# Performance work log

Measured on AMD Instinct MI355X. Metric: run time of the kernel, lower is better.

The kernel has to match this reference:

```python
import jax, jax.numpy as jnp
import numpy as np

N = 100000        # nodes
E = 1600000       # edges (avg degree 16)
IN_DIM = 128
OUT_DIM = 128
P_DROP = 0.1


def setup_inputs() -> dict:
    key = jax.random.key(0)
    k1, k2, k3, k4 = jax.random.split(key, 4)
    x = jax.random.normal(k1, (N, IN_DIM), dtype=jnp.float32)
    edge_index = jax.random.randint(k2, (2, E), 0, N, dtype=jnp.int64)
    # glorot-uniform-ish init for the GCNConv linear weight
    limit = float(np.sqrt(6.0 / (IN_DIM + OUT_DIM)))
    W = jax.random.uniform(k3, (IN_DIM, OUT_DIM), dtype=jnp.float32,
                           minval=-limit, maxval=limit)
    b = jnp.zeros((OUT_DIM,), dtype=jnp.float32)
    drop_u = jax.random.uniform(k4, (N, OUT_DIM), dtype=jnp.float32)
    return {"x": x, "edge_index": edge_index, "W": W, "b": b, "drop_u": drop_u}


def reference(x, edge_index, W, b, drop_u):
    n = x.shape[0]
    # linear transform first (PyG GCNConv: lin has no bias)
    h = x @ W  # [N, OUT]
    # add self-loops
    loops = jnp.arange(n, dtype=edge_index.dtype)
    src = jnp.concatenate([edge_index[0], loops])  # [E+N]
    dst = jnp.concatenate([edge_index[1], loops])
    # symmetric normalization: deg computed on destination column
    deg = jax.ops.segment_sum(jnp.ones_like(dst, dtype=h.dtype), dst,
                              num_segments=n)
    dinv = jnp.where(deg > 0, jax.lax.rsqrt(deg), 0.0)
    norm = dinv[src] * dinv[dst]  # [E+N]
    # gather-message-scatter: out[dst] += norm * h[src]
    msgs = h[src] * norm[:, None]                       # [E+N, OUT]
    out = jax.ops.segment_sum(msgs, dst, num_segments=n) + b
    # ReLU + (deterministic-mask) inverted dropout
    out = jax.nn.relu(out)
    keep = 1.0 - P_DROP
    out = jnp.where(drop_u >= P_DROP, out / keep, 0.0)
    return out
```

## Files before the change

### kernel.cpp

```cpp
#include <hip/hip_runtime.h>

#define DIM 128
#define D4 32
#define D2 64
#define EPB1 4096

typedef short short8 __attribute__((ext_vector_type(8)));
typedef float f32x4 __attribute__((ext_vector_type(4)));

__device__ __forceinline__ unsigned pack_bf16(float a, float b) {
    unsigned ua = __float_as_uint(a);
    unsigned ub = __float_as_uint(b);
    ua = (ua + 0x7FFFu + ((ua >> 16) & 1u)) >> 16;
    ub = (ub + 0x7FFFu + ((ub >> 16) & 1u)) & 0xFFFF0000u;
    return ua | ub;
}
__device__ __forceinline__ unsigned short bf16_of(float a) {
    unsigned ua = __float_as_uint(a);
    return (unsigned short)((ua + 0x7FFFu + ((ua >> 16) & 1u)) >> 16);
}


__global__ __launch_bounds__(512) void k_hist1(const int* __restrict__ dst, int E,
                                               int* __restrict__ H, int* __restrict__ tot,
                                               int NB1, int NBUCK) {
    __shared__ int h[512];
    const int t = threadIdx.x;
    for (int i = t; i < NBUCK; i += 512) h[i] = 0;
    __syncthreads();
    const int base = blockIdx.x * EPB1;
#pragma unroll
    for (int i = 0; i < EPB1 / 512; ++i) {
        int e = base + i * 512 + t;
        if (e < E) atomicAdd(&h[dst[e] >> 9], 1);
    }
    __syncthreads();
    for (int i = t; i < NBUCK; i += 512) {
        int c = h[i];
        H[i * NB1 + blockIdx.x] = c;
        if (c) atomicAdd(&tot[i], c);
    }
}

__global__ __launch_bounds__(512) void k_scanA(const int* __restrict__ tot,
                                               int* __restrict__ binbase, int NBUCK) {
    __shared__ int sh[512];
    const int t = threadIdx.x;
    int v = (t < NBUCK) ? tot[t] : 0;
    sh[t] = v;
    __syncthreads();
    for (int o = 1; o < 512; o <<= 1) {
        int x = (t >= o) ? sh[t - o] : 0;
        __syncthreads();
        sh[t] += x;
        __syncthreads();
    }
    if (t < NBUCK) binbase[t] = sh[t] - v;
    if (t == NBUCK - 1) binbase[NBUCK] = sh[t];
}

__global__ __launch_bounds__(512) void k_scanB(int* __restrict__ H,
                                               const int* __restrict__ binbase, int NB1) {
    __shared__ int sh[512];
    const int bin = blockIdx.x;
    const int t = threadIdx.x;
    int v = (t < NB1) ? H[bin * NB1 + t] : 0;
    sh[t] = v;
    __syncthreads();
    for (int o = 1; o < 512; o <<= 1) {
        int x = (t >= o) ? sh[t - o] : 0;
        __syncthreads();
        sh[t] += x;
        __syncthreads();
    }
    if (t < NB1) H[bin * NB1 + t] = binbase[bin] + sh[t] - v;
}

__global__ __launch_bounds__(512) void k_scatter1(const int* __restrict__ ei, int E,
                                                  const int* __restrict__ H,
                                                  unsigned* __restrict__ ebuf,
                                                  int NB1, int NBUCK) {
    __shared__ int cnt[512];
    const int t = threadIdx.x;
    const int blk = blockIdx.x;
    for (int i = t; i < NBUCK; i += 512) cnt[i] = 0;
    __syncthreads();
    const int* src = ei;
    const int* dst = ei + E;
    const int base = blk * EPB1;
#pragma unroll
    for (int i = 0; i < EPB1 / 512; ++i) {
        int e = base + i * 512 + t;
        if (e < E) {
            int d = dst[e];
            int s = src[e];
            int b = d >> 9;
            int r = atomicAdd(&cnt[b], 1);
            ebuf[H[b * NB1 + blk] + r] = ((unsigned)s << 9) | (unsigned)(d & 511);
        }
    }
}

__global__ __launch_bounds__(512) void k_bucket2(const unsigned* __restrict__ ebuf,
                                                 const int* __restrict__ binbase,
                                                 int* __restrict__ srclist,
                                                 int* __restrict__ rowstart,
                                                 float* __restrict__ dinv,
                                                 int n, int E) {
    __shared__ int h[512];
    __shared__ int off[512];
    __shared__ int cnt[512];
    const int t = threadIdx.x;
    const int b = blockIdx.x;
    const int beg = binbase[b];
    const int end = binbase[b + 1];
    h[t] = 0; cnt[t] = 0;
    __syncthreads();
    for (int j = beg + t; j < end; j += 512) atomicAdd(&h[ebuf[j] & 511], 1);
    __syncthreads();
    int v = h[t];
    off[t] = v;
    __syncthreads();
    for (int o = 1; o < 512; o <<= 1) {
        int x = (t >= o) ? off[t - o] : 0;
        __syncthreads();
        off[t] += x;
        __syncthreads();
    }
    const int excl = off[t] - v;
    const int node = b * 512 + t;
    if (node < n) {
        rowstart[node] = beg + excl;
        dinv[node] = rsqrtf((float)(v + 1));
    }
    if (b == 0 && t == 0) rowstart[n] = E;
    h[t] = beg + excl;
    __syncthreads();
    for (int j = beg + t; j < end; j += 512) {
        unsigned p = ebuf[j];
        int lo = p & 511;
        int r = atomicAdd(&cnt[lo], 1);
        srclist[h[lo] + r] = (int)(p >> 9);
    }
}


__global__ __launch_bounds__(256) void k_xprep(const float* __restrict__ x,
                                               const float* __restrict__ dinv,
                                               unsigned* __restrict__ xs, int n) {
    long t = (long)blockIdx.x * blockDim.x + threadIdx.x;
    long total = (long)n * D4;
    if (t >= total) return;
    int row = (int)(t >> 5);
    float di = dinv[row];
    float4 v = ((const float4*)x)[t];
    uint2 o;
    o.x = pack_bf16(v.x * di, v.y * di);
    o.y = pack_bf16(v.z * di, v.w * di);
    ((uint2*)xs)[t] = o;
}

__global__ __launch_bounds__(256) void k_wprep(const float* __restrict__ W,
                                               unsigned short* __restrict__ wt) {
    int o = blockIdx.x * blockDim.x + threadIdx.x;
    if (o >= DIM * DIM) return;
    int j = o >> 7, k = o & 127;
    wt[o] = bf16_of(W[k * DIM + j]);
}

__global__ __launch_bounds__(256) void k_gather_bb(const int* __restrict__ rowstart,
                                                   const int* __restrict__ srclist,
                                                   const unsigned* __restrict__ xs,
                                                   const float* __restrict__ dinv,
                                                   unsigned* __restrict__ agg, int n) {
    const int node = blockIdx.x * 4 + (threadIdx.x >> 6);
    const int lane = threadIdx.x & 63;
    if (node >= n) return;
    const float di = dinv[node];

    unsigned sv = xs[(long)node * D2 + lane];
    float2 acc;
    acc.x = __uint_as_float(sv << 16);
    acc.y = __uint_as_float(sv & 0xFFFF0000u);

    const int beg = rowstart[node];
    const int end = rowstart[node + 1];
    int j = beg;
    for (; j + 3 < end; j += 4) {
        int s0 = srclist[j];
        int s1 = srclist[j + 1];
        int s2 = srclist[j + 2];
        int s3 = srclist[j + 3];
        unsigned v0 = xs[(long)s0 * D2 + lane];
        unsigned v1 = xs[(long)s1 * D2 + lane];
        unsigned v2 = xs[(long)s2 * D2 + lane];
        unsigned v3 = xs[(long)s3 * D2 + lane];
        acc.x += __uint_as_float(v0 << 16) + __uint_as_float(v1 << 16)
               + __uint_as_float(v2 << 16) + __uint_as_float(v3 << 16);
        acc.y += __uint_as_float(v0 & 0xFFFF0000u) + __uint_as_float(v1 & 0xFFFF0000u)
               + __uint_as_float(v2 & 0xFFFF0000u) + __uint_as_float(v3 & 0xFFFF0000u);
    }
    for (; j < end; ++j) {
        unsigned v0 = xs[(long)srclist[j] * D2 + lane];
        acc.x += __uint_as_float(v0 << 16);
        acc.y += __uint_as_float(v0 & 0xFFFF0000u);
    }
    agg[(long)node * D2 + lane] = pack_bf16(acc.x * di, acc.y * di);
}

__global__ __launch_bounds__(256) void k_mfma_transform(
        const unsigned short* __restrict__ A,
        const unsigned short* __restrict__ WT,
        const float* __restrict__ bias,
        const float* __restrict__ du,
        float* __restrict__ out, int n, int ntiles) {
    const int wave  = threadIdx.x >> 6;
    const int lane  = threadIdx.x & 63;
    const int rhalf = wave >> 1;
    const int cg    = wave & 1;
    const int lr    = lane & 15;
    const int lk8   = (lane >> 4) * 8;

    short8 bfr[4][4];
    float  bcol[4];
#pragma unroll
    for (int ct = 0; ct < 4; ++ct) {
        int col = cg * 64 + ct * 16 + lr;
        bcol[ct] = bias[col];
#pragma unroll
        for (int ks = 0; ks < 4; ++ks)
            bfr[ct][ks] = *reinterpret_cast<const short8*>(WT + col * DIM + ks * 32 + lk8);
    }

    for (int t = blockIdx.x; t < ntiles; t += gridDim.x) {
        const long row0 = (long)t * 32 + rhalf * 16;
        long ar = row0 + lr; if (ar >= n) ar = n - 1;
        short8 afr[4];
#pragma unroll
        for (int ks = 0; ks < 4; ++ks)
            afr[ks] = *reinterpret_cast<const short8*>(A + ar * DIM + ks * 32 + lk8);

#pragma unroll
        for (int ct = 0; ct < 4; ++ct) {
            f32x4 acc = {0.f, 0.f, 0.f, 0.f};
#pragma unroll
            for (int ks = 0; ks < 4; ++ks)
                acc = __builtin_amdgcn_mfma_f32_16x16x32_bf16(afr[ks], bfr[ct][ks], acc, 0, 0, 0);
            const int gcol = cg * 64 + ct * 16 + lr;
            const long rbase = row0 + (lane >> 4) * 4;
#pragma unroll
            for (int r = 0; r < 4; ++r) {
                long grow = rbase + r;
                if (grow < n) {
                    float v = acc[r] + bcol[ct];
                    float u = du[grow * DIM + gcol];
                    v = (u >= 0.1f) ? fmaxf(v, 0.f) * (1.0f / 0.9f) : 0.f;
                    out[grow * DIM + gcol] = v;
                }
            }
        }
    }
}


__global__ void k_hist(const int* __restrict__ dst, int E, int* __restrict__ hist) {
    int e = blockIdx.x * blockDim.x + threadIdx.x;
    if (e < E) atomicAdd(&hist[dst[e]], 1);
}
__global__ void k_dinv(const int* __restrict__ hist, float* __restrict__ dinv, int n) {
    int i = blockIdx.x * blockDim.x + threadIdx.x;
    if (i < n) dinv[i] = rsqrtf((float)(hist[i] + 1));
}
__global__ __launch_bounds__(256) void k_scan1(const int* __restrict__ hist,
                                               int* __restrict__ rowstart,
                                               int* __restrict__ bsum, int n) {
    __shared__ int sh[256];
    const int t = threadIdx.x;
    const int base = blockIdx.x * 1024 + t * 4;
    int v0 = (base + 0 < n) ? hist[base + 0] : 0;
    int v1 = (base + 1 < n) ? hist[base + 1] : 0;
    int v2 = (base + 2 < n) ? hist[base + 2] : 0;
    int v3 = (base + 3 < n) ? hist[base + 3] : 0;
    int s = v0 + v1 + v2 + v3;
    sh[t] = s;
    __syncthreads();
    for (int off = 1; off < 256; off <<= 1) {
        int xv = (t >= off) ? sh[t - off] : 0;
        __syncthreads();
        sh[t] += xv;
        __syncthreads();
    }
    if (t == 255) bsum[blockIdx.x] = sh[255];
    int run = sh[t] - s;
    if (base + 0 < n) rowstart[base + 0] = run; run += v0;
    if (base + 1 < n) rowstart[base + 1] = run; run += v1;
    if (base + 2 < n) rowstart[base + 2] = run; run += v2;
    if (base + 3 < n) rowstart[base + 3] = run;
}
__global__ __launch_bounds__(256) void k_scan2(int* __restrict__ bsum, int B) {
    __shared__ int sh[256];
    const int t = threadIdx.x;
    int v = (t < B) ? bsum[t] : 0;
    sh[t] = v;
    __syncthreads();
    for (int off = 1; off < 256; off <<= 1) {
        int xv = (t >= off) ? sh[t - off] : 0;
        __syncthreads();
        sh[t] += xv;
        __syncthreads();
    }
    if (t < B) bsum[t] = sh[t] - v;
}
__global__ void k_scan3(int* __restrict__ rowstart, const int* __restrict__ bsum,
                        int n, int E) {
    int i = blockIdx.x * blockDim.x + threadIdx.x;
    if (i < n) rowstart[i] += bsum[i >> 10];
    else if (i == n) rowstart[n] = E;
}
__global__ void k_fill(const int* __restrict__ ei, int E,
                       const int* __restrict__ rowstart, int* __restrict__ cursor,
                       int* __restrict__ srclist) {
    int e = blockIdx.x * blockDim.x + threadIdx.x;
    if (e >= E) return;
    int d = ei[E + e];
    int pos = atomicAdd(&cursor[d], 1);
    srclist[rowstart[d] + pos] = ei[e];
}
__global__ __launch_bounds__(256) void k_gather_bf(const int* __restrict__ rowstart,
                                                   const int* __restrict__ srclist,
                                                   const unsigned* __restrict__ xs,
                                                   const float* __restrict__ dinv,
                                                   float* __restrict__ out, int n) {
    const int node = blockIdx.x * 4 + (threadIdx.x >> 6);
    const int lane = threadIdx.x & 63;
    if (node >= n) return;
    const float di = dinv[node];
    unsigned sv = xs[(long)node * D2 + lane];
    float2 acc;
    acc.x = __uint_as_float(sv << 16);
    acc.y = __uint_as_float(sv & 0xFFFF0000u);
    const int beg = rowstart[node];
    const int end = rowstart[node + 1];
    int j = beg;
    for (; j + 3 < end; j += 4) {
        int s0 = srclist[j]; int s1 = srclist[j + 1];
        int s2 = srclist[j + 2]; int s3 = srclist[j + 3];
        unsigned v0 = xs[(long)s0 * D2 + lane];
        unsigned v1 = xs[(long)s1 * D2 + lane];
        unsigned v2 = xs[(long)s2 * D2 + lane];
        unsigned v3 = xs[(long)s3 * D2 + lane];
        acc.x += __uint_as_float(v0 << 16) + __uint_as_float(v1 << 16)
               + __uint_as_float(v2 << 16) + __uint_as_float(v3 << 16);
        acc.y += __uint_as_float(v0 & 0xFFFF0000u) + __uint_as_float(v1 & 0xFFFF0000u)
               + __uint_as_float(v2 & 0xFFFF0000u) + __uint_as_float(v3 & 0xFFFF0000u);
    }
    for (; j < end; ++j) {
        unsigned v0 = xs[(long)srclist[j] * D2 + lane];
        acc.x += __uint_as_float(v0 << 16);
        acc.y += __uint_as_float(v0 & 0xFFFF0000u);
    }
    acc.x *= di; acc.y *= di;
    ((float2*)out)[(long)node * D2 + lane] = acc;
}
#define RPG 8
__global__ __launch_bounds__(256, 5) void k_transform(
        float* __restrict__ io, const float* __restrict__ W,
        const float* __restrict__ bias, const float* __restrict__ du, int n) {
    __shared__ float4 Wl[64 * D4];
    const float4* W4 = (const float4*)W;
    const int l = threadIdx.x & 31;
    const int g = threadIdx.x >> 5;
    const float4 bb = ((const float4*)bias)[l];
    const float inv_keep = 1.0f / 0.9f;
    long r0 = (long)blockIdx.x * 64 + (long)g * RPG;
    float4 acc[RPG];
#pragma unroll
    for (int r = 0; r < RPG; ++r) acc[r] = make_float4(0.f, 0.f, 0.f, 0.f);
    for (int half = 0; half < 2; ++half) {
        __syncthreads();
        for (int i = threadIdx.x; i < 64 * D4; i += 256)
            Wl[i] = W4[half * 64 * D4 + i];
        __syncthreads();
        const int kb = half * 16;
#pragma unroll 4
        for (int k4 = 0; k4 < 16; ++k4) {
            float4 w0 = Wl[(k4 * 4 + 0) * D4 + l];
            float4 w1 = Wl[(k4 * 4 + 1) * D4 + l];
            float4 w2 = Wl[(k4 * 4 + 2) * D4 + l];
            float4 w3 = Wl[(k4 * 4 + 3) * D4 + l];
#pragma unroll
            for (int r = 0; r < RPG; ++r) {
                long row = r0 + r;
                if (row < n) {
                    float4 a = ((const float4*)io)[row * D4 + kb + k4];
                    acc[r].x += a.x * w0.x + a.y * w1.x + a.z * w2.x + a.w * w3.x;
                    acc[r].y += a.x * w0.y + a.y * w1.y + a.z * w2.y + a.w * w3.y;
                    acc[r].z += a.x * w0.z + a.y * w1.z + a.z * w2.z + a.w * w3.z;
                    acc[r].w += a.x * w0.w + a.y * w1.w + a.z * w2.w + a.w * w3.w;
                }
            }
        }
    }
#pragma unroll
    for (int r = 0; r < RPG; ++r) {
        long row = r0 + r;
        if (row < n) {
            float4 v = acc[r];
            v.x += bb.x; v.y += bb.y; v.z += bb.z; v.w += bb.w;
            float4 u = ((const float4*)du)[row * D4 + l];
            v.x = (u.x >= 0.1f) ? fmaxf(v.x, 0.f) * inv_keep : 0.f;
            v.y = (u.y >= 0.1f) ? fmaxf(v.y, 0.f) * inv_keep : 0.f;
            v.z = (u.z >= 0.1f) ? fmaxf(v.z, 0.f) * inv_keep : 0.f;
            v.w = (u.w >= 0.1f) ? fmaxf(v.w, 0.f) * inv_keep : 0.f;
            ((float4*)io)[row * D4 + l] = v;
        }
    }
}

extern "C" void kernel_launch(void* const* d_in, const int* in_sizes, int n_in,
                              void* d_out, int out_size, void* d_ws, size_t ws_size,
                              hipStream_t stream) {
    const float* x  = (const float*)d_in[0];
    const int*   ei = (const int*)d_in[1];
    const float* W  = (const float*)d_in[2];
    const float* b  = (const float*)d_in[3];
    const float* du = (const float*)d_in[4];
    float* out = (float*)d_out;

    const int n = in_sizes[0] / DIM;
    const int E = in_sizes[1] / 2;

    auto al = [](size_t v) { return (v + 255) & ~(size_t)255; };
    char* ws = (char*)d_ws;

    const int NBUCK = (n + 511) >> 9;
    const int NB1   = (E + EPB1 - 1) / EPB1;

    size_t o_dinv = 0;
    size_t o_rs   = o_dinv + al((size_t)n * 4);
    size_t o_src  = o_rs   + al(((size_t)n + 1) * 4);
    size_t o_xs   = o_src  + al((size_t)E * 4);
    size_t o_agg  = o_xs   + al((size_t)n * DIM * 2);
    size_t o_wt   = o_agg  + al((size_t)n * DIM * 2);
    size_t o_H    = o_wt   + al((size_t)DIM * DIM * 2);
    size_t o_tot  = o_H    + al((size_t)NBUCK * NB1 * 4);
    size_t o_bb   = o_tot  + al((size_t)NBUCK * 4);
    size_t o_ebuf = o_bb   + al(((size_t)NBUCK + 1) * 4);
    size_t need3  = o_ebuf + (size_t)E * 4;

    float* dinv     = (float*)(ws + o_dinv);
    int*   rowstart = (int*)(ws + o_rs);
    int*   srclist  = (int*)(ws + o_src);
    unsigned* xs    = (unsigned*)(ws + o_xs);
    unsigned* agg   = (unsigned*)(ws + o_agg);
    unsigned short* wt = (unsigned short*)(ws + o_wt);
    int*   H        = (int*)(ws + o_H);
    int*   tot      = (int*)(ws + o_tot);
    int*   binbase  = (int*)(ws + o_bb);
    unsigned* ebuf  = (unsigned*)(ws + o_ebuf);

    const int bs = 256;

    if (ws_size >= need3 && NBUCK <= 512 && NB1 <= 512) {
        hipMemsetAsync(tot, 0, (size_t)NBUCK * 4, stream);
        k_hist1<<<NB1, 512, 0, stream>>>(ei + E, E, H, tot, NB1, NBUCK);
        k_scanA<<<1, 512, 0, stream>>>(tot, binbase, NBUCK);
        k_scanB<<<NBUCK, 512, 0, stream>>>(H, binbase, NB1);
        k_scatter1<<<NB1, 512, 0, stream>>>(ei, E, H, ebuf, NB1, NBUCK);
        k_bucket2<<<NBUCK, 512, 0, stream>>>(ebuf, binbase, srclist, rowstart, dinv, n, E);

        long t_x = (long)n * D4;
        k_xprep<<<(int)((t_x + bs - 1) / bs), bs, 0, stream>>>(x, dinv, xs, n);
        k_wprep<<<(DIM * DIM + bs - 1) / bs, bs, 0, stream>>>(W, wt);
        k_gather_bb<<<(n + 3) / 4, 256, 0, stream>>>(rowstart, srclist, xs, dinv, agg, n);
        int ntiles = (n + 31) / 32;
        int grid = ntiles < 1024 ? ntiles : 1024;
        k_mfma_transform<<<grid, 256, 0, stream>>>((const unsigned short*)agg, wt,
                                                   b, du, out, n, ntiles);
        return;
    }

    size_t f_dinv = 0;
    size_t f_hist = f_dinv + al((size_t)n * 4);
    size_t f_rs   = f_hist + al((size_t)n * 4);
    size_t f_bsum = f_rs   + al(((size_t)n + 1) * 4);
    size_t f_src  = f_bsum + 1024;
    size_t f_xs   = f_src  + al((size_t)E * 4);
    size_t f_agg  = f_xs   + al((size_t)n * DIM * 2);
    size_t f_wt   = f_agg  + al((size_t)n * DIM * 2);
    size_t need1  = f_agg;
    size_t need2  = f_wt + (size_t)DIM * DIM * 2;

    float* fdinv     = (float*)(ws + f_dinv);
    int*   fhist     = (int*)(ws + f_hist);
    int*   frowstart = (int*)(ws + f_rs);
    int*   fbsum     = (int*)(ws + f_bsum);
    int*   fsrclist  = (int*)(ws + f_src);
    unsigned* fxs    = (unsigned*)(ws + f_xs);
    unsigned* fagg   = (unsigned*)(ws + f_agg);
    unsigned short* fwt = (unsigned short*)(ws + f_wt);

    const int B = (n + 1023) / 1024;
    hipMemsetAsync(fhist, 0, (size_t)n * 4, stream);
    k_hist<<<(E + bs - 1) / bs, bs, 0, stream>>>(ei + E, E, fhist);
    k_dinv<<<(n + bs - 1) / bs, bs, 0, stream>>>(fhist, fdinv, n);
    k_scan1<<<B, 256, 0, stream>>>(fhist, frowstart, fbsum, n);
    k_scan2<<<1, 256, 0, stream>>>(fbsum, B);
    k_scan3<<<(n + 1 + bs - 1) / bs, bs, 0, stream>>>(frowstart, fbsum, n, E);
    hipMemsetAsync(fhist, 0, (size_t)n * 4, stream);
    k_fill<<<(E + bs - 1) / bs, bs, 0, stream>>>(ei, E, frowstart, fhist, fsrclist);

    if (ws_size >= need2) {
        long t_x = (long)n * D4;
        k_xprep<<<(int)((t_x + bs - 1) / bs), bs, 0, stream>>>(x, fdinv, fxs, n);
        k_wprep<<<(DIM * DIM + bs - 1) / bs, bs, 0, stream>>>(W, fwt);
        k_gather_bb<<<(n + 3) / 4, 256, 0, stream>>>(frowstart, fsrclist, fxs, fdinv, fagg, n);
        int ntiles = (n + 31) / 32;
        int grid = ntiles < 1024 ? ntiles : 1024;
        k_mfma_transform<<<grid, 256, 0, stream>>>((const unsigned short*)fagg, fwt,
                                                   b, du, out, n, ntiles);
    } else if (ws_size >= need1) {
        long t_x = (long)n * D4;
        k_xprep<<<(int)((t_x + bs - 1) / bs), bs, 0, stream>>>(x, fdinv, fxs, n);
        k_gather_bf<<<(n + 3) / 4, 256, 0, stream>>>(frowstart, fsrclist, fxs, fdinv, out, n);
        int blocks_t = (int)((n + 63) / 64);
        k_transform<<<blocks_t, 256, 0, stream>>>(out, W, b, du, n);
    }
}
```

Baseline: 175.9 us.

## Fold W prep and bucket scan into existing kernels; shuffle-broadcast gather indices

The W transpose/bf16 conversion moves into extra blocks of the histogram kernel, and the single-block bucket-total scan is merged into k_scanB, where every block redundantly rescans the totals. Together these drop two kernel launches. The gather kernel now loads up to 64 source indices per wave in one coalesced read and broadcasts them with __shfl, replacing per-edge scalar index loads. The cost is redundant scan work in every scanB block and extra shuffle instructions in the gather loop.

```diff
diff --git a/kernel.cpp b/kernel.cpp
--- a/kernel.cpp
+++ b/kernel.cpp
@@ -23,7 +23,21 @@
 
 __global__ __launch_bounds__(512) void k_hist1(const int* __restrict__ dst, int E,
                                                int* __restrict__ H, int* __restrict__ tot,
-                                               int NB1, int NBUCK) {
+                                               int NB1, int NBUCK,
+                                               const float* __restrict__ W,
+                                               unsigned short* __restrict__ wt) {
+    if (blockIdx.x >= (unsigned)NB1) {
+        int base = (blockIdx.x - NB1) * 2048 + threadIdx.x * 4;
+#pragma unroll
+        for (int i = 0; i < 4; ++i) {
+            int o = base + i;
+            if (o < DIM * DIM) {
+                int j = o >> 7, k = o & 127;
+                wt[o] = bf16_of(W[k * DIM + j]);
+            }
+        }
+        return;
+    }
     __shared__ int h[512];
     const int t = threadIdx.x;
     for (int i = t; i < NBUCK; i += 512) h[i] = 0;
@@ -42,28 +56,28 @@
     }
 }
 
-__global__ __launch_bounds__(512) void k_scanA(const int* __restrict__ tot,
-                                               int* __restrict__ binbase, int NBUCK) {
-    __shared__ int sh[512];
-    const int t = threadIdx.x;
-    int v = (t < NBUCK) ? tot[t] : 0;
-    sh[t] = v;
-    __syncthreads();
-    for (int o = 1; o < 512; o <<= 1) {
-        int x = (t >= o) ? sh[t - o] : 0;
-        __syncthreads();
-        sh[t] += x;
-        __syncthreads();
-    }
-    if (t < NBUCK) binbase[t] = sh[t] - v;
-    if (t == NBUCK - 1) binbase[NBUCK] = sh[t];
-}
-
 __global__ __launch_bounds__(512) void k_scanB(int* __restrict__ H,
-                                               const int* __restrict__ binbase, int NB1) {
+                                               const int* __restrict__ tot,
+                                               int* __restrict__ binbase,
+                                               int NB1, int NBUCK, int E) {
     __shared__ int sh[512];
     const int bin = blockIdx.x;
     const int t = threadIdx.x;
+
+    int tv = (t < NBUCK) ? tot[t] : 0;
+    sh[t] = tv;
+    __syncthreads();
+    for (int o = 1; o < 512; o <<= 1) {
+        int x = (t >= o) ? sh[t - o] : 0;
+        __syncthreads();
+        sh[t] += x;
+        __syncthreads();
+    }
+    const int mybase = sh[bin] - ((bin < NBUCK) ? tot[bin] : 0);
+    if (t == bin && t < NBUCK) binbase[t] = mybase;
+    if (bin == 0 && t == 0) binbase[NBUCK] = E;
+    __syncthreads();
+
     int v = (t < NB1) ? H[bin * NB1 + t] : 0;
     sh[t] = v;
     __syncthreads();
@@ -73,7 +87,7 @@
         sh[t] += x;
         __syncthreads();
     }
-    if (t < NB1) H[bin * NB1 + t] = binbase[bin] + sh[t] - v;
+    if (t < NB1) H[bin * NB1 + t] = mybase + sh[t] - v;
 }
 
 __global__ __launch_bounds__(512) void k_scatter1(const int* __restrict__ ei, int E,
@@ -179,33 +193,38 @@
     const float di = dinv[node];
 
     unsigned sv = xs[(long)node * D2 + lane];
-    float2 acc;
-    acc.x = __uint_as_float(sv << 16);
-    acc.y = __uint_as_float(sv & 0xFFFF0000u);
+    float ax = __uint_as_float(sv << 16);
+    float ay = __uint_as_float(sv & 0xFFFF0000u);
 
     const int beg = rowstart[node];
     const int end = rowstart[node + 1];
-    int j = beg;
-    for (; j + 3 < end; j += 4) {
-        int s0 = srclist[j];
-        int s1 = srclist[j + 1];
-        int s2 = srclist[j + 2];
-        int s3 = srclist[j + 3];
-        unsigned v0 = xs[(long)s0 * D2 + lane];
-        unsigned v1 = xs[(long)s1 * D2 + lane];
-        unsigned v2 = xs[(long)s2 * D2 + lane];
-        unsigned v3 = xs[(long)s3 * D2 + lane];
-        acc.x += __uint_as_float(v0 << 16) + __uint_as_float(v1 << 16)
-               + __uint_as_float(v2 << 16) + __uint_as_float(v3 << 16);
-        acc.y += __uint_as_float(v0 & 0xFFFF0000u) + __uint_as_float(v1 & 0xFFFF0000u)
-               + __uint_as_float(v2 & 0xFFFF0000u) + __uint_as_float(v3 & 0xFFFF0000u);
-    }
-    for (; j < end; ++j) {
-        unsigned v0 = xs[(long)srclist[j] * D2 + lane];
-        acc.x += __uint_as_float(v0 << 16);
-        acc.y += __uint_as_float(v0 & 0xFFFF0000u);
-    }
-    agg[(long)node * D2 + lane] = pack_bf16(acc.x * di, acc.y * di);
+    for (int base = beg; base < end; base += 64) {
+        const int m = (end - base < 64) ? (end - base) : 64;
+        int sidx = 0;
+        if (base + lane < end) sidx = srclist[base + lane];
+        int k = 0;
+        for (; k + 3 < m; k += 4) {
+            int s0 = __shfl(sidx, k);
+            int s1 = __shfl(sidx, k + 1);
+            int s2 = __shfl(sidx, k + 2);
+            int s3 = __shfl(sidx, k + 3);
+            unsigned v0 = xs[(long)s0 * D2 + lane];
+            unsigned v1 = xs[(long)s1 * D2 + lane];
+            unsigned v2 = xs[(long)s2 * D2 + lane];
+            unsigned v3 = xs[(long)s3 * D2 + lane];
+            ax += __uint_as_float(v0 << 16) + __uint_as_float(v1 << 16)
+                + __uint_as_float(v2 << 16) + __uint_as_float(v3 << 16);
+            ay += __uint_as_float(v0 & 0xFFFF0000u) + __uint_as_float(v1 & 0xFFFF0000u)
+                + __uint_as_float(v2 & 0xFFFF0000u) + __uint_as_float(v3 & 0xFFFF0000u);
+        }
+        for (; k < m; ++k) {
+            int s = __shfl(sidx, k);
+            unsigned v = xs[(long)s * D2 + lane];
+            ax += __uint_as_float(v << 16);
+            ay += __uint_as_float(v & 0xFFFF0000u);
+        }
+    }
+    agg[(long)node * D2 + lane] = pack_bf16(ax * di, ay * di);
 }
 
 __global__ __launch_bounds__(256) void k_mfma_transform(
@@ -463,15 +482,13 @@
 
     if (ws_size >= need3 && NBUCK <= 512 && NB1 <= 512) {
         hipMemsetAsync(tot, 0, (size_t)NBUCK * 4, stream);
-        k_hist1<<<NB1, 512, 0, stream>>>(ei + E, E, H, tot, NB1, NBUCK);
-        k_scanA<<<1, 512, 0, stream>>>(tot, binbase, NBUCK);
-        k_scanB<<<NBUCK, 512, 0, stream>>>(H, binbase, NB1);
+        k_hist1<<<NB1 + 8, 512, 0, stream>>>(ei + E, E, H, tot, NB1, NBUCK, W, wt);
+        k_scanB<<<NBUCK, 512, 0, stream>>>(H, tot, binbase, NB1, NBUCK, E);
         k_scatter1<<<NB1, 512, 0, stream>>>(ei, E, H, ebuf, NB1, NBUCK);
         k_bucket2<<<NBUCK, 512, 0, stream>>>(ebuf, binbase, srclist, rowstart, dinv, n, E);
 
         long t_x = (long)n * D4;
         k_xprep<<<(int)((t_x + bs - 1) / bs), bs, 0, stream>>>(x, dinv, xs, n);
-        k_wprep<<<(DIM * DIM + bs - 1) / bs, bs, 0, stream>>>(W, wt);
         k_gather_bb<<<(n + 3) / 4, 256, 0, stream>>>(rowstart, srclist, xs, dinv, agg, n);
         int ntiles = (n + 31) / 32;
         int grid = ntiles < 1024 ? ntiles : 1024;
```

Measured after the change: 162.7 us. 1.08x faster.
